# Kernel optimization log

Measured on AMD Instinct MI355X. Metric: run time of the kernel, lower is better.

Reference implementation:

```python
import jax, jax.numpy as jnp
import numpy as np

NHEADS = 2
STRENGTH = 0.1
ZED = 8  # zone_embed_dim
STATE_DIM = 137
HID = 256
NBLOCKS = 4
BATCH = 131072


def _mha_seq1(q, k, v, in_w, in_b, out_w, out_b):
    """nn.MultiheadAttention (batch_first) with q,k,v of shape [B,1,E]."""
    B, _, E = q.shape
    hd = E // NHEADS
    Wq, Wk, Wv = in_w[:E], in_w[E:2 * E], in_w[2 * E:]
    bq, bk, bv = in_b[:E], in_b[E:2 * E], in_b[2 * E:]

    def heads(x, W, b):
        return (x @ W.T + b).reshape(B, -1, NHEADS, hd).transpose(0, 2, 1, 3)  # [B,H,1,hd]

    qh, kh, vh = heads(q, Wq, bq), heads(k, Wk, bk), heads(v, Wv, bv)
    scale = 1.0 / jnp.sqrt(jnp.asarray(hd, q.dtype))
    s = jnp.einsum('bhqd,bhkd->bhqk', qh, kh) * scale
    a = jax.nn.softmax(s, axis=-1)  # trivially ones for kv_len=1, kept for fidelity
    o = jnp.einsum('bhqk,bhkd->bhqd', a, vh).transpose(0, 2, 1, 3).reshape(B, -1, E)
    return o @ out_w.T + out_b


def setup_inputs() -> dict:
    key = jax.random.key(0)
    ks = jax.random.split(key, 20)
    S, H, N = STATE_DIM, HID, NBLOCKS
    ahd = S - ZED - 1  # 128

    def w(k, shape, fan_in):
        return jax.random.normal(k, shape, jnp.float32) * (1.0 / np.sqrt(fan_in))

    inp = {
        't': jax.random.uniform(ks[0], (1,), jnp.float32) * 24.0,
        'state': jax.random.normal(ks[1], (BATCH, S), jnp.float32),
        'W0': w(ks[2], (H, S + 2), S + 2), 'b0': jnp.zeros((H,), jnp.float32),
        'blkW1': w(ks[3], (N, H, H), H), 'blkb1': jnp.zeros((N, H), jnp.float32),
        'blkW2': w(ks[4], (N, H, H), H), 'blkb2': jnp.zeros((N, H), jnp.float32),
        'Wout': w(ks[5], (S, H), H), 'bout': jnp.zeros((S,), jnp.float32),
        'lm_in_w': w(ks[6], (3 * ZED, ZED), ZED), 'lm_in_b': jnp.zeros((3 * ZED,), jnp.float32),
        'lm_out_w': w(ks[7], (ZED, ZED), ZED), 'lm_out_b': jnp.zeros((ZED,), jnp.float32),
        'ta_in_w': w(ks[8], (3 * ahd, ahd), ahd), 'ta_in_b': jnp.zeros((3 * ahd,), jnp.float32),
        'ta_out_w': w(ks[9], (ahd, ahd), ahd), 'ta_out_b': jnp.zeros((ahd,), jnp.float32),
    }
    return inp


def reference(t, state, W0, b0, blkW1, blkb1, blkW2, blkb2, Wout, bout,
              lm_in_w, lm_in_b, lm_out_w, lm_out_b,
              ta_in_w, ta_in_b, ta_out_w, ta_out_b):
    B, S = state.shape
    ahd = S - ZED - 1
    two_pi_over_24 = 2.0 * jnp.pi / 24.0
    tv = jnp.concatenate([jnp.sin(t * two_pi_over_24), jnp.cos(t * two_pi_over_24)])  # [2]
    t_vec = jnp.broadcast_to(tv, (B, 2))

    # core dynamics MLP: Linear -> ReLU -> residual blocks -> Linear
    x = jnp.concatenate([state, t_vec], axis=-1)
    h = jax.nn.relu(x @ W0.T + b0)
    for i in range(blkW1.shape[0]):
        inner = jnp.tanh(h @ blkW1[i].T + blkb1[i]) @ blkW2[i].T + blkb2[i]
        h = jnp.tanh(h + inner)
    core = h @ Wout.T + bout

    # attention delta
    hs = state[:, :ahd]
    loc = state[:, ahd:ahd + ZED]
    mov = state[:, -1:]

    q_lm = jnp.broadcast_to(mov, (B, ZED))[:, None, :]
    loc_e = loc[:, None, :]
    enh_loc = _mha_seq1(q_lm, loc_e, loc_e, lm_in_w, lm_in_b, lm_out_w, lm_out_b)[:, 0]
    delta_loc = enh_loc - loc

    t_pad = jnp.concatenate([t_vec, jnp.zeros((B, ahd - 2), state.dtype)], axis=-1)[:, None, :]
    h_e = hs[:, None, :]
    enh_h = _mha_seq1(t_pad, h_e, h_e, ta_in_w, ta_in_b, ta_out_w, ta_out_b)[:, 0]
    delta_h = enh_h - hs

    delta = jnp.concatenate([delta_h, delta_loc, jnp.zeros_like(mov)], axis=-1)
    return core + STRENGTH * delta
```

## Files before the change

kernel.cpp:

```cpp
#include <hip/hip_runtime.h>

typedef __attribute__((ext_vector_type(8))) short short8;
typedef __attribute__((ext_vector_type(4))) float float4_;

#define SDIM    137
#define HID     256
#define K0PAD   160
#define KAUG    416
#define MTILE   128
#define NROWT   (MTILE / 16)
#define NTHR    512

#define SCLF 2.8853900817779268f
#define ISCL 0.34657359027997264f

struct __attribute__((aligned(8))) U2 { unsigned x, y; };

__device__ __forceinline__ unsigned short f2bf(float f) {
  union { float f; unsigned int i; } v; v.f = f;
  return (unsigned short)((v.i + 0x8000u) >> 16);
}
__device__ __forceinline__ unsigned pack_bf16(float a, float b) {
  union { float f; unsigned u; } ua, ub; ua.f = a; ub.f = b;
  return __builtin_amdgcn_perm(ub.u + 0x8000u, ua.u + 0x8000u, 0x07060302u);
}
__device__ __forceinline__ unsigned cvt_pk(float a, float b) {
  unsigned r;
  asm("v_cvt_pk_bf16_f32 %0, %1, %2" : "=v"(r) : "v"(a), "v"(b));
  return r;
}
__device__ __forceinline__ float lo_bf(unsigned p) {
  union { unsigned u; float f; } v; v.u = p << 16; return v.f;
}
__device__ __forceinline__ float hi_bf(unsigned p) {
  union { unsigned u; float f; } v; v.u = p & 0xFFFF0000u; return v.f;
}
__device__ __forceinline__ float stanh(float y) {
#if __has_builtin(__builtin_amdgcn_exp2f)
  float e = __builtin_amdgcn_exp2f(y);
#else
  float e = __expf(y * 0.6931471805599453f);
#endif
  float r = __builtin_amdgcn_rcpf(e + 1.f);
  return __builtin_fmaf(-2.f * SCLF, r, SCLF);
}
__device__ __forceinline__ int sidx(int row, int col) {
  return row * 256 + ((((col >> 3) ^ (row & 31)) << 3) | (col & 7));
}
__device__ __forceinline__ short8 ld_x(const unsigned short* __restrict__ X, int row, int c) {
  return *(const short8*)(X + row * 256 + (((c ^ (row & 31)) << 3)));
}

template<int NK, int LDB, int BOFF>
__device__ __forceinline__ void load_wa(const unsigned short* __restrict__ W,
                                        short8 (&wa)[NK][2], int colbase, int rm, int q)
{
  #pragma unroll
  for (int kb = 0; kb < NK; ++kb)
    #pragma unroll
    for (int mt = 0; mt < 2; ++mt)
      wa[kb][mt] = *(const short8*)(W + (size_t)(colbase + mt * 16 + rm) * LDB
                                      + BOFF + kb * 32 + q * 8);
}

template<int NK, class EPI>
__device__ __forceinline__ void gemm_f(const unsigned short* __restrict__ X,
                                       const short8 (&wa)[NK][2],
                                       int rm, int q, EPI epi)
{
  float4_ a[NROWT][2];
  #pragma unroll
  for (int nt = 0; nt < NROWT; ++nt) {
    short8 xb[NK];
    #pragma unroll
    for (int kb = 0; kb < NK; ++kb) xb[kb] = ld_x(X, nt * 16 + rm, kb * 4 + q);
    a[nt][0] = (float4_){0.f, 0.f, 0.f, 0.f};
    a[nt][1] = (float4_){0.f, 0.f, 0.f, 0.f};
    #pragma unroll
    for (int kb = 0; kb < NK; ++kb) {
      a[nt][0] = __builtin_amdgcn_mfma_f32_16x16x32_bf16(wa[kb][0], xb[kb], a[nt][0], 0, 0, 0);
      a[nt][1] = __builtin_amdgcn_mfma_f32_16x16x32_bf16(wa[kb][1], xb[kb], a[nt][1], 0, 0, 0);
    }
    if (nt > 0) epi(nt - 1, a[nt - 1]);
  }
  epi(NROWT - 1, a[NROWT - 1]);
}

template<int NK, int LDB, int BOFF>
__device__ __forceinline__ void mma_wact(const unsigned short* __restrict__ X,
                                         const unsigned short* __restrict__ W,
                                         float4_ (&acc)[2][NROWT], int lane, int colbase)
{
  const int q  = lane >> 4;
  const int rm = lane & 15;
  short8 wa[NK][2];
  load_wa<NK, LDB, BOFF>(W, wa, colbase, rm, q);
  #pragma unroll
  for (int kb = 0; kb < NK; ++kb) {
    short8 xb[NROWT];
    #pragma unroll
    for (int nt = 0; nt < NROWT; ++nt)
      xb[nt] = ld_x(X, nt * 16 + rm, kb * 4 + q);
    #pragma unroll
    for (int mt = 0; mt < 2; ++mt)
      #pragma unroll
      for (int nt = 0; nt < NROWT; ++nt)
        acc[mt][nt] = __builtin_amdgcn_mfma_f32_16x16x32_bf16(wa[kb][mt], xb[nt], acc[mt][nt], 0, 0, 0);
  }
}


__global__ void prep_w0(const float* __restrict__ t,
                        const float* __restrict__ W0,
                        const float* __restrict__ b0,
                        unsigned short* __restrict__ W0p,
                        float* __restrict__ b0p)
{
  int n = blockIdx.x;
  int tt = threadIdx.x;
  for (int k = tt; k < K0PAD; k += 64)
    W0p[n * K0PAD + k] = (k < SDIM) ? f2bf(W0[n * 139 + k] * SCLF) : (unsigned short)0;
  if (tt == 0) {
    float tv  = t[0];
    float ang = tv * (6.2831853071795864f / 24.0f);
    float sv = __sinf(ang), cv = __cosf(ang);
    b0p[n] = SCLF * (b0[n] + W0[n * 139 + 137] * sv + W0[n * 139 + 138] * cv);
  }
}

__global__ void prep_fill(const float* __restrict__ Wout,
                          const float* __restrict__ bout,
                          unsigned short* __restrict__ Waug,
                          float* __restrict__ baug)
{
  int n = blockIdx.x;
  int tt = threadIdx.x;
  if (tt < KAUG / 4) {
    int k0 = tt * 4;
    U2 p;
    if (k0 < 256 && n < SDIM) {
      float4_ v = *(const float4_*)(Wout + (size_t)n * 256 + k0);
      p.x = pack_bf16(v[0] * ISCL, v[1] * ISCL); p.y = pack_bf16(v[2] * ISCL, v[3] * ISCL);
    } else {
      p.x = 0u; p.y = 0u;
    }
    *(U2*)(Waug + (size_t)n * KAUG + k0) = p;
  } else if (tt == KAUG / 4) {
    baug[n] = (n < SDIM) ? bout[n] : 0.f;
  }
}

__global__ void prep_ta(const float* __restrict__ ta_in_w,
                        const float* __restrict__ ta_in_b,
                        const float* __restrict__ ta_out_w,
                        const float* __restrict__ ta_out_b,
                        const float* __restrict__ lm_in_w,
                        const float* __restrict__ lm_in_b,
                        const float* __restrict__ lm_out_w,
                        const float* __restrict__ lm_out_b,
                        unsigned short* __restrict__ Waug,
                        float* __restrict__ baug)
{
  __shared__ float red[128];
  int blk = blockIdx.x;
  int tt  = threadIdx.x;
  if (blk < 128) {
    int n = blk, s = tt;
    float dot = 0.f;
    #pragma unroll 8
    for (int r = 0; r < 128; ++r)
      dot += ta_out_w[n * 128 + r] * ta_in_w[(256 + r) * 128 + s];
    float v = 0.1f * (dot - (s == n ? 1.f : 0.f));
    Waug[(size_t)n * KAUG + 256 + s] = f2bf(v);

    red[tt] = ta_out_w[n * 128 + tt] * ta_in_b[256 + tt];
    __syncthreads();
    if (tt < 64) {
      float p = red[tt] + red[tt + 64];
      for (int off = 32; off; off >>= 1) p += __shfl_down(p, off);
      if (tt == 0) baug[n] += 0.1f * (p + ta_out_b[n]);
    }
  } else {
    if (tt < 64) {
      int a = tt >> 3, b = tt & 7;
      float dot = 0.f;
      #pragma unroll
      for (int r = 0; r < 8; ++r)
        dot += lm_out_w[a * 8 + r] * lm_in_w[(16 + r) * 8 + b];
      Waug[(size_t)(128 + a) * KAUG + 384 + b] = f2bf(0.1f * (dot - (a == b ? 1.f : 0.f)));
    } else if (tt < 72) {
      int a = tt - 64;
      float dot = 0.f;
      #pragma unroll
      for (int r = 0; r < 8; ++r)
        dot += lm_out_w[a * 8 + r] * lm_in_b[16 + r];
      baug[128 + a] += 0.1f * (dot + lm_out_b[a]);
    }
  }
}

__global__ void prep_blk2(const float* __restrict__ s1, const float* __restrict__ s2,
                          unsigned short* __restrict__ d1, unsigned short* __restrict__ d2)
{
  int i = (blockIdx.x * 256 + threadIdx.x) * 4;
  const float* s; unsigned short* d;
  if (i < 262144) { s = s1 + i;          d = d1 + i; }
  else            { s = s2 + i - 262144; d = d2 + i - 262144; }
  float4_ v = *(const float4_*)s;
  U2 p; p.x = pack_bf16(v[0], v[1]); p.y = pack_bf16(v[2], v[3]);
  *(U2*)d = p;
}


__global__ __launch_bounds__(NTHR, 2)
__attribute__((amdgpu_waves_per_eu(2, 2)))
void fused_odefunc(
    const float* __restrict__ state,
    const unsigned short* __restrict__ W0p,
    const float* __restrict__ b0p,
    const unsigned short* __restrict__ blkW1,
    const float* __restrict__ blkb1,
    const unsigned short* __restrict__ blkW2,
    const float* __restrict__ blkb2,
    const unsigned short* __restrict__ Waug,
    const float* __restrict__ baug,
    float* __restrict__ out)
{
  __shared__ __align__(16) unsigned short ARENA[2 * MTILE * 256];
  unsigned short* H = ARENA;
  unsigned short* G = ARENA + MTILE * 256;
  float*          T = (float*)ARENA;

  const int tid  = threadIdx.x;
  const int lane = tid & 63;
  const int wave = tid >> 6;
  const int q    = lane >> 4;
  const int rm   = lane & 15;
  const int cb   = wave * 32;
  const int row0 = blockIdx.x * MTILE;

  #pragma unroll 2
  for (int qd = tid; qd < MTILE * (K0PAD / 4); qd += NTHR) {
    int m  = qd / (K0PAD / 4);
    int k0 = (qd - m * (K0PAD / 4)) * 4;
    const float* sp = state + (size_t)(row0 + m) * SDIM + k0;
    float f0 = (k0     < SDIM) ? sp[0] : 0.f;
    float f1 = (k0 + 1 < SDIM) ? sp[1] : 0.f;
    float f2 = (k0 + 2 < SDIM) ? sp[2] : 0.f;
    float f3 = (k0 + 3 < SDIM) ? sp[3] : 0.f;
    U2 p; p.x = cvt_pk(f0, f1); p.y = cvt_pk(f2, f3);
    *(U2*)(&G[sidx(m, k0)]) = p;
  }
  __syncthreads();

  {
    short8 wa[K0PAD / 32][2];
    load_wa<K0PAD / 32, K0PAD, 0>(W0p, wa, cb, rm, q);
    float4_ bias[2];
    #pragma unroll
    for (int mt = 0; mt < 2; ++mt) bias[mt] = *(const float4_*)(b0p + cb + mt * 16 + q * 4);
    gemm_f<K0PAD / 32>(G, wa, rm, q, [&](int nt, float4_ (&a2)[2]) {
      int row = nt * 16 + rm;
      #pragma unroll
      for (int mt = 0; mt < 2; ++mt) {
        int col0 = cb + mt * 16 + q * 4;
        float v0 = fmaxf(a2[mt][0] + bias[mt][0], 0.f);
        float v1 = fmaxf(a2[mt][1] + bias[mt][1], 0.f);
        float v2 = fmaxf(a2[mt][2] + bias[mt][2], 0.f);
        float v3 = fmaxf(a2[mt][3] + bias[mt][3], 0.f);
        U2 p; p.x = cvt_pk(v0, v1); p.y = cvt_pk(v2, v3);
        *(U2*)(&H[sidx(row, col0)]) = p;
      }
    });
  }
  __syncthreads();

  for (int blk = 0; blk < 4; ++blk) {
    const unsigned short* W1 = blkW1 + (size_t)blk * 65536;
    const float*          b1 = blkb1 + blk * 256;
    const unsigned short* W2 = blkW2 + (size_t)blk * 65536;
    const float*          b2 = blkb2 + blk * 256;

    {
      short8 wa[8][2];
      load_wa<8, 256, 0>(W1, wa, cb, rm, q);
      float4_ bb[2];
      #pragma unroll
      for (int mt = 0; mt < 2; ++mt) {
        float4_ t4 = *(const float4_*)(b1 + cb + mt * 16 + q * 4);
        bb[mt][0] = t4[0] * SCLF; bb[mt][1] = t4[1] * SCLF;
        bb[mt][2] = t4[2] * SCLF; bb[mt][3] = t4[3] * SCLF;
      }
      gemm_f<8>(H, wa, rm, q, [&](int nt, float4_ (&a2)[2]) {
        int row = nt * 16 + rm;
        #pragma unroll
        for (int mt = 0; mt < 2; ++mt) {
          int col0 = cb + mt * 16 + q * 4;
          float g0 = stanh(a2[mt][0] + bb[mt][0]);
          float g1 = stanh(a2[mt][1] + bb[mt][1]);
          float g2 = stanh(a2[mt][2] + bb[mt][2]);
          float g3 = stanh(a2[mt][3] + bb[mt][3]);
          U2 p; p.x = cvt_pk(g0, g1); p.y = cvt_pk(g2, g3);
          *(U2*)(&G[sidx(row, col0)]) = p;
        }
      });
    }
    __syncthreads();

    {
      short8 wa[8][2];
      load_wa<8, 256, 0>(W2, wa, cb, rm, q);
      float4_ bb[2];
      #pragma unroll
      for (int mt = 0; mt < 2; ++mt) {
        float4_ t4 = *(const float4_*)(b2 + cb + mt * 16 + q * 4);
        bb[mt][0] = t4[0] * SCLF; bb[mt][1] = t4[1] * SCLF;
        bb[mt][2] = t4[2] * SCLF; bb[mt][3] = t4[3] * SCLF;
      }
      gemm_f<8>(G, wa, rm, q, [&](int nt, float4_ (&a2)[2]) {
        int row = nt * 16 + rm;
        #pragma unroll
        for (int mt = 0; mt < 2; ++mt) {
          int col0 = cb + mt * 16 + q * 4;
          int idx = sidx(row, col0);
          U2 old = *(const U2*)(&H[idx]);
          float h0 = stanh(lo_bf(old.x) + a2[mt][0] + bb[mt][0]);
          float h1 = stanh(hi_bf(old.x) + a2[mt][1] + bb[mt][1]);
          float h2 = stanh(lo_bf(old.y) + a2[mt][2] + bb[mt][2]);
          float h3 = stanh(hi_bf(old.y) + a2[mt][3] + bb[mt][3]);
          U2 p; p.x = cvt_pk(h0, h1); p.y = cvt_pk(h2, h3);
          *(U2*)(&H[idx]) = p;
        }
      });
    }
    __syncthreads();
  }

  #pragma unroll 2
  for (int qd = tid; qd < MTILE * (K0PAD / 4); qd += NTHR) {
    int m  = qd / (K0PAD / 4);
    int k0 = (qd - m * (K0PAD / 4)) * 4;
    const float* sp = state + (size_t)(row0 + m) * SDIM + k0;
    float f0 = (k0     < SDIM) ? sp[0] : 0.f;
    float f1 = (k0 + 1 < SDIM) ? sp[1] : 0.f;
    float f2 = (k0 + 2 < SDIM) ? sp[2] : 0.f;
    float f3 = (k0 + 3 < SDIM) ? sp[3] : 0.f;
    U2 p; p.x = cvt_pk(f0, f1); p.y = cvt_pk(f2, f3);
    *(U2*)(&G[sidx(m, k0)]) = p;
  }

  float4_ acc[2][NROWT];
  #pragma unroll
  for (int mt = 0; mt < 2; ++mt)
    #pragma unroll
    for (int nt = 0; nt < NROWT; ++nt) acc[mt][nt] = (float4_){0.f, 0.f, 0.f, 0.f};
  if (cb < 160)
    mma_wact<8, KAUG, 0>(H, Waug, acc, lane, cb);
  __syncthreads();
  if (cb < 160)
    mma_wact<5, KAUG, 256>(G, Waug, acc, lane, cb);
  __syncthreads();
  if (cb < 160) {
    #pragma unroll
    for (int mt = 0; mt < 2; ++mt) {
      int col0 = cb + mt * 16 + q * 4;
      if (col0 <= 136) {
        float4_ bias = *(const float4_*)(baug + col0);
        #pragma unroll
        for (int nt = 0; nt < NROWT; ++nt) {
          int row = nt * 16 + rm;
          float4_ v;
          v[0] = acc[mt][nt][0] + bias[0];
          v[1] = acc[mt][nt][1] + bias[1];
          v[2] = acc[mt][nt][2] + bias[2];
          v[3] = acc[mt][nt][3] + bias[3];
          *(float4_*)(T + row * 140 + col0) = v;
        }
      }
    }
  }
  __syncthreads();

  float* obase = out + (size_t)row0 * SDIM;
  int r = tid / SDIM;
  int c = tid - r * SDIM;
  #pragma unroll 1
  for (int idx = tid; idx < MTILE * SDIM; idx += NTHR) {
    obase[idx] = T[r * 140 + c];
    c += NTHR - 3 * SDIM;
    r += 3;
    if (c >= SDIM) { c -= SDIM; r += 1; }
  }
}

extern "C" void kernel_launch(void* const* d_in, const int* in_sizes, int n_in,
                              void* d_out, int out_size, void* d_ws, size_t ws_size,
                              hipStream_t stream) {
  const float* t        = (const float*)d_in[0];
  const float* state    = (const float*)d_in[1];
  const float* W0       = (const float*)d_in[2];
  const float* b0       = (const float*)d_in[3];
  const float* blkW1    = (const float*)d_in[4];
  const float* blkb1    = (const float*)d_in[5];
  const float* blkW2    = (const float*)d_in[6];
  const float* blkb2    = (const float*)d_in[7];
  const float* Wout     = (const float*)d_in[8];
  const float* bout     = (const float*)d_in[9];
  const float* lm_in_w  = (const float*)d_in[10];
  const float* lm_in_b  = (const float*)d_in[11];
  const float* lm_out_w = (const float*)d_in[12];
  const float* lm_out_b = (const float*)d_in[13];
  const float* ta_in_w  = (const float*)d_in[14];
  const float* ta_in_b  = (const float*)d_in[15];
  const float* ta_out_w = (const float*)d_in[16];
  const float* ta_out_b = (const float*)d_in[17];

  char* ws = (char*)d_ws;
  unsigned short* W0p   = (unsigned short*)ws;
  float*          b0p   = (float*)(ws + 81920);
  unsigned short* Waug  = (unsigned short*)(ws + 82944);
  float*          baug  = (float*)(ws + 295936);
  unsigned short* W1b   = (unsigned short*)(ws + 296960);
  unsigned short* W2b   = (unsigned short*)(ws + 821248);

  prep_w0<<<256, 64, 0, stream>>>(t, W0, b0, W0p, b0p);
  prep_fill<<<256, 128, 0, stream>>>(Wout, bout, Waug, baug);
  prep_ta<<<129, 128, 0, stream>>>(ta_in_w, ta_in_b, ta_out_w, ta_out_b,
                                   lm_in_w, lm_in_b, lm_out_w, lm_out_b, Waug, baug);
  prep_blk2<<<512, 256, 0, stream>>>(blkW1, blkW2, W1b, W2b);

  int batch = in_sizes[1] / SDIM;
  fused_odefunc<<<batch / MTILE, NTHR, 0, stream>>>(
      state, W0p, b0p, W1b, blkb1, W2b, blkb2, Waug, baug,
      (float*)d_out);
}
```

Measured before the change: 456.6 us.

## Halve row tile, raise occupancy, and merge weight-prep kernels into one launch

Reduces the per-block row tile from 128 to 64, halving LDS use so more blocks and waves can reside per CU, and relaxes launch bounds to four blocks per CU. The four weight-preparation kernels are merged into a single launch with block-range dispatch, writing biases directly instead of accumulating across kernels. The smaller tile lowers weight reuse per row and the tighter register budget risks spills.

```diff
diff --git a/kernel.cpp b/kernel.cpp
--- a/kernel.cpp
+++ b/kernel.cpp
@@ -7,7 +7,7 @@
 #define HID     256
 #define K0PAD   160
 #define KAUG    416
-#define MTILE   128
+#define MTILE   64
 #define NROWT   (MTILE / 16)
 #define NTHR    512
 
@@ -109,111 +109,103 @@
   }
 }
 
-
-__global__ void prep_w0(const float* __restrict__ t,
-                        const float* __restrict__ W0,
-                        const float* __restrict__ b0,
-                        unsigned short* __restrict__ W0p,
-                        float* __restrict__ b0p)
+#define PB_TA   256
+#define PB_W0   385
+#define PB_BLK  641
+#define PB_END  1665
+
+__global__ void prep_all(const float* __restrict__ t,
+                         const float* __restrict__ W0,  const float* __restrict__ b0,
+                         const float* __restrict__ Wout,const float* __restrict__ bout,
+                         const float* __restrict__ lm_in_w, const float* __restrict__ lm_in_b,
+                         const float* __restrict__ lm_out_w,const float* __restrict__ lm_out_b,
+                         const float* __restrict__ ta_in_w, const float* __restrict__ ta_in_b,
+                         const float* __restrict__ ta_out_w,const float* __restrict__ ta_out_b,
+                         const float* __restrict__ blkW1, const float* __restrict__ blkW2,
+                         unsigned short* __restrict__ W0p,  float* __restrict__ b0p,
+                         unsigned short* __restrict__ Waug, float* __restrict__ baug,
+                         unsigned short* __restrict__ W1b,  unsigned short* __restrict__ W2b)
 {
-  int n = blockIdx.x;
-  int tt = threadIdx.x;
-  for (int k = tt; k < K0PAD; k += 64)
-    W0p[n * K0PAD + k] = (k < SDIM) ? f2bf(W0[n * 139 + k] * SCLF) : (unsigned short)0;
-  if (tt == 0) {
-    float tv  = t[0];
-    float ang = tv * (6.2831853071795864f / 24.0f);
-    float sv = __sinf(ang), cv = __cosf(ang);
-    b0p[n] = SCLF * (b0[n] + W0[n * 139 + 137] * sv + W0[n * 139 + 138] * cv);
-  }
-}
-
-__global__ void prep_fill(const float* __restrict__ Wout,
-                          const float* __restrict__ bout,
-                          unsigned short* __restrict__ Waug,
-                          float* __restrict__ baug)
-{
-  int n = blockIdx.x;
-  int tt = threadIdx.x;
-  if (tt < KAUG / 4) {
-    int k0 = tt * 4;
-    U2 p;
-    if (k0 < 256 && n < SDIM) {
-      float4_ v = *(const float4_*)(Wout + (size_t)n * 256 + k0);
-      p.x = pack_bf16(v[0] * ISCL, v[1] * ISCL); p.y = pack_bf16(v[2] * ISCL, v[3] * ISCL);
+  const int blk = blockIdx.x;
+  const int tt  = threadIdx.x;
+
+  if (blk < PB_TA) {
+    int n = blk;
+    if (tt < KAUG / 4) {
+      int k0 = tt * 4;
+      bool patch = (k0 >= 256) && ((n < 128 && k0 < 384) ||
+                                   (n >= 128 && n < 136 && k0 >= 384 && k0 < 392));
+      if (!patch) {
+        U2 p;
+        if (k0 < 256 && n < SDIM) {
+          float4_ v = *(const float4_*)(Wout + (size_t)n * 256 + k0);
+          p.x = pack_bf16(v[0] * ISCL, v[1] * ISCL);
+          p.y = pack_bf16(v[2] * ISCL, v[3] * ISCL);
+        } else { p.x = 0u; p.y = 0u; }
+        *(U2*)(Waug + (size_t)n * KAUG + k0) = p;
+      }
+    }
+  } else if (blk < PB_W0) {
+    int b = blk - PB_TA;
+    if (b < 128) {
+      __shared__ float red[128];
+      int n = b, s = tt;
+      float dot = 0.f;
+      #pragma unroll 8
+      for (int r = 0; r < 128; ++r)
+        dot += ta_out_w[n * 128 + r] * ta_in_w[(256 + r) * 128 + s];
+      Waug[(size_t)n * KAUG + 256 + s] = f2bf(0.1f * (dot - (s == n ? 1.f : 0.f)));
+
+      red[tt] = ta_out_w[n * 128 + tt] * ta_in_b[256 + tt];
+      __syncthreads();
+      if (tt < 64) {
+        float p = red[tt] + red[tt + 64];
+        for (int off = 32; off; off >>= 1) p += __shfl_down(p, off);
+        if (tt == 0) baug[n] = bout[n] + 0.1f * (p + ta_out_b[n]);
+      }
     } else {
-      p.x = 0u; p.y = 0u;
-    }
-    *(U2*)(Waug + (size_t)n * KAUG + k0) = p;
-  } else if (tt == KAUG / 4) {
-    baug[n] = (n < SDIM) ? bout[n] : 0.f;
-  }
-}
-
-__global__ void prep_ta(const float* __restrict__ ta_in_w,
-                        const float* __restrict__ ta_in_b,
-                        const float* __restrict__ ta_out_w,
-                        const float* __restrict__ ta_out_b,
-                        const float* __restrict__ lm_in_w,
-                        const float* __restrict__ lm_in_b,
-                        const float* __restrict__ lm_out_w,
-                        const float* __restrict__ lm_out_b,
-                        unsigned short* __restrict__ Waug,
-                        float* __restrict__ baug)
-{
-  __shared__ float red[128];
-  int blk = blockIdx.x;
-  int tt  = threadIdx.x;
-  if (blk < 128) {
-    int n = blk, s = tt;
-    float dot = 0.f;
-    #pragma unroll 8
-    for (int r = 0; r < 128; ++r)
-      dot += ta_out_w[n * 128 + r] * ta_in_w[(256 + r) * 128 + s];
-    float v = 0.1f * (dot - (s == n ? 1.f : 0.f));
-    Waug[(size_t)n * KAUG + 256 + s] = f2bf(v);
-
-    red[tt] = ta_out_w[n * 128 + tt] * ta_in_b[256 + tt];
-    __syncthreads();
-    if (tt < 64) {
-      float p = red[tt] + red[tt + 64];
-      for (int off = 32; off; off >>= 1) p += __shfl_down(p, off);
-      if (tt == 0) baug[n] += 0.1f * (p + ta_out_b[n]);
+      if (tt < 64) {
+        int a = tt >> 3, c = tt & 7;
+        float dot = 0.f;
+        #pragma unroll
+        for (int r = 0; r < 8; ++r)
+          dot += lm_out_w[a * 8 + r] * lm_in_w[(16 + r) * 8 + c];
+        Waug[(size_t)(128 + a) * KAUG + 384 + c] = f2bf(0.1f * (dot - (a == c ? 1.f : 0.f)));
+      } else if (tt < 72) {
+        int a = tt - 64;
+        float dot = 0.f;
+        #pragma unroll
+        for (int r = 0; r < 8; ++r)
+          dot += lm_out_w[a * 8 + r] * lm_in_b[16 + r];
+        baug[128 + a] = bout[128 + a] + 0.1f * (dot + lm_out_b[a]);
+      } else if (tt == 72) {
+        baug[136] = bout[136];
+        baug[137] = 0.f; baug[138] = 0.f; baug[139] = 0.f;
+      }
+    }
+  } else if (blk < PB_BLK) {
+    int n = blk - PB_W0;
+    for (int k = tt; k < K0PAD; k += 128)
+      W0p[n * K0PAD + k] = (k < SDIM) ? f2bf(W0[n * 139 + k] * SCLF) : (unsigned short)0;
+    if (tt == 0) {
+      float tv  = t[0];
+      float ang = tv * (6.2831853071795864f / 24.0f);
+      float sv = __sinf(ang), cv = __cosf(ang);
+      b0p[n] = SCLF * (b0[n] + W0[n * 139 + 137] * sv + W0[n * 139 + 138] * cv);
     }
   } else {
-    if (tt < 64) {
-      int a = tt >> 3, b = tt & 7;
-      float dot = 0.f;
-      #pragma unroll
-      for (int r = 0; r < 8; ++r)
-        dot += lm_out_w[a * 8 + r] * lm_in_w[(16 + r) * 8 + b];
-      Waug[(size_t)(128 + a) * KAUG + 384 + b] = f2bf(0.1f * (dot - (a == b ? 1.f : 0.f)));
-    } else if (tt < 72) {
-      int a = tt - 64;
-      float dot = 0.f;
-      #pragma unroll
-      for (int r = 0; r < 8; ++r)
-        dot += lm_out_w[a * 8 + r] * lm_in_b[16 + r];
-      baug[128 + a] += 0.1f * (dot + lm_out_b[a]);
-    }
-  }
-}
-
-__global__ void prep_blk2(const float* __restrict__ s1, const float* __restrict__ s2,
-                          unsigned short* __restrict__ d1, unsigned short* __restrict__ d2)
-{
-  int i = (blockIdx.x * 256 + threadIdx.x) * 4;
-  const float* s; unsigned short* d;
-  if (i < 262144) { s = s1 + i;          d = d1 + i; }
-  else            { s = s2 + i - 262144; d = d2 + i - 262144; }
-  float4_ v = *(const float4_*)s;
-  U2 p; p.x = pack_bf16(v[0], v[1]); p.y = pack_bf16(v[2], v[3]);
-  *(U2*)d = p;
-}
-
-
-__global__ __launch_bounds__(NTHR, 2)
-__attribute__((amdgpu_waves_per_eu(2, 2)))
+    int i = ((blk - PB_BLK) * 128 + tt) * 4;
+    const float* s; unsigned short* d;
+    if (i < 262144) { s = blkW1 + i;          d = W1b + i; }
+    else            { s = blkW2 + i - 262144; d = W2b + i - 262144; }
+    float4_ v = *(const float4_*)s;
+    U2 p; p.x = pack_bf16(v[0], v[1]); p.y = pack_bf16(v[2], v[3]);
+    *(U2*)d = p;
+  }
+}
+
+
+__global__ __launch_bounds__(NTHR, 4)
 void fused_odefunc(
     const float* __restrict__ state,
     const unsigned short* __restrict__ W0p,
@@ -423,11 +415,11 @@
   unsigned short* W1b   = (unsigned short*)(ws + 296960);
   unsigned short* W2b   = (unsigned short*)(ws + 821248);
 
-  prep_w0<<<256, 64, 0, stream>>>(t, W0, b0, W0p, b0p);
-  prep_fill<<<256, 128, 0, stream>>>(Wout, bout, Waug, baug);
-  prep_ta<<<129, 128, 0, stream>>>(ta_in_w, ta_in_b, ta_out_w, ta_out_b,
-                                   lm_in_w, lm_in_b, lm_out_w, lm_out_b, Waug, baug);
-  prep_blk2<<<512, 256, 0, stream>>>(blkW1, blkW2, W1b, W2b);
+  prep_all<<<PB_END, 128, 0, stream>>>(t, W0, b0, Wout, bout,
+                                       lm_in_w, lm_in_b, lm_out_w, lm_out_b,
+                                       ta_in_w, ta_in_b, ta_out_w, ta_out_b,
+                                       blkW1, blkW2,
+                                       W0p, b0p, Waug, baug, W1b, W2b);
 
   int batch = in_sizes[1] / SDIM;
   fused_odefunc<<<batch / MTILE, NTHR, 0, stream>>>(
```

Result: slower. 478.6 us (+4.8%).
